# Kernel tuning notes

Hardware: AMD Instinct MI355X
Metric: run time of the kernel (lower is better)

Reference implementation:

```python
import jax, jax.numpy as jnp
import numpy as np


def setup_inputs() -> dict:
    key = jax.random.key(0)
    k1, k2 = jax.random.split(key)
    B, C, H, W = 32, 256, 64, 64
    data = jax.random.normal(k1, (B, C, H, W), dtype=jnp.float32)
    offset = jax.random.normal(k2, (B, 2, H, W), dtype=jnp.float32)
    trans_std = jnp.float32(0.005)  # learned scalar Parameter
    return {"data": data, "offset": offset, "trans_std": trans_std}


def reference(data, offset, trans_std):
    """Offset-driven bilinear interpolation sampling + global average pooling.

    data:   [B, C, H, W]
    offset: [B, 2, H, W]  (dy, dx) displacement field, scaled by trans_std
    Returns pooled features [B, C].
    """
    B, C, H, W = data.shape
    ts = jnp.clip(trans_std, 0.001, 0.01)  # forward clamps trans_std to [0.001, 0.01]

    # sampling coordinates: base grid + scaled offsets (offsets normalized by H/W)
    ii = jnp.arange(H, dtype=data.dtype)[:, None]   # [H,1]
    jj = jnp.arange(W, dtype=data.dtype)[None, :]   # [1,W]
    y = jnp.clip(ii + ts * offset[:, 0] * H, 0.0, H - 1)  # [B,H,W]
    x = jnp.clip(jj + ts * offset[:, 1] * W, 0.0, W - 1)  # [B,H,W]

    y0 = jnp.clip(jnp.floor(y).astype(jnp.int32), 0, H - 2)
    x0 = jnp.clip(jnp.floor(x).astype(jnp.int32), 0, W - 2)
    y1 = y0 + 1
    x1 = x0 + 1
    wy = y - y0.astype(data.dtype)  # [B,H,W] in [0,1]
    wx = x - x0.astype(data.dtype)

    def sample_one(d, yy0, yy1, xx0, xx1):
        # d: [C,H,W]; index maps: [H,W] -> gathered [C,H,W]
        v00 = d[:, yy0, xx0]
        v01 = d[:, yy0, xx1]
        v10 = d[:, yy1, xx0]
        v11 = d[:, yy1, xx1]
        return v00, v01, v10, v11

    v00, v01, v10, v11 = jax.vmap(sample_one)(data, y0, y1, x0, x1)  # each [B,C,H,W]

    wy_ = wy[:, None]  # broadcast over channels -> [B,1,H,W]
    wx_ = wx[:, None]
    sampled = ((1 - wy_) * (1 - wx_) * v00 + (1 - wy_) * wx_ * v01
               + wy_ * (1 - wx_) * v10 + wy_ * wx_ * v11)  # [B,C,H,W]

    # pooling: global average over spatial locations -> [B,C]
    return jnp.mean(sampled, axis=(2, 3))
```

## Files before the change

### kernel.cpp

```cpp
#include <hip/hip_runtime.h>

#define BATCH 32
#define CHAN  256
#define HGT   64
#define WID   64
#define HW    4096

__global__ __launch_bounds__(256) void weight_map_kernel(
        const float* __restrict__ offset,
        const float* __restrict__ ts_ptr,
        float* __restrict__ A)
{
    const int b   = blockIdx.x;
    const int tid = threadIdx.x;

    __shared__ float acc[HW];
    for (int k = tid; k < HW; k += 256) acc[k] = 0.0f;
    __syncthreads();

    float ts = ts_ptr[0];
    ts = fminf(fmaxf(ts, 0.001f), 0.01f);

    const float* off_y = offset + (size_t)b * 2 * HW;
    const float* off_x = off_y + HW;

    for (int p = tid; p < HW; p += 256) {
        const int i = p >> 6;
        const int j = p & 63;
        const float dy = off_y[p];
        const float dx = off_x[p];
        float y = fminf(fmaxf((float)i + ts * dy * 64.0f, 0.0f), 63.0f);
        float x = fminf(fmaxf((float)j + ts * dx * 64.0f, 0.0f), 63.0f);
        int y0 = (int)floorf(y); y0 = min(max(y0, 0), HGT - 2);
        int x0 = (int)floorf(x); x0 = min(max(x0, 0), WID - 2);
        const float wy = y - (float)y0;
        const float wx = x - (float)x0;
        const int base = (y0 << 6) + x0;
        atomicAdd(&acc[base],           (1.0f - wy) * (1.0f - wx));
        atomicAdd(&acc[base + 1],       (1.0f - wy) * wx);
        atomicAdd(&acc[base + WID],     wy * (1.0f - wx));
        atomicAdd(&acc[base + WID + 1], wy * wx);
    }
    __syncthreads();

    float* Ab = A + (size_t)b * HW;
    const float s = 1.0f / (float)HW;
    for (int k = tid; k < HW; k += 256) Ab[k] = acc[k] * s;
}

__global__ __launch_bounds__(256) void dot_kernel(
        const float* __restrict__ data,
        const float* __restrict__ A,
        float* __restrict__ out)
{
    const int blk = blockIdx.x;
    const int b   = blk >> 8;
    const int tid = threadIdx.x;

    const float* plane = data + (size_t)blk * HW;
    const float* Ab    = A    + (size_t)b   * HW;

    float sum = 0.0f;
    #pragma unroll
    for (int it = 0; it < 4; ++it) {
        const int idx = (it * 256 + tid) * 4;
        const float4 dv = *reinterpret_cast<const float4*>(plane + idx);
        const float4 av = *reinterpret_cast<const float4*>(Ab + idx);
        sum = fmaf(av.x, dv.x, sum);
        sum = fmaf(av.y, dv.y, sum);
        sum = fmaf(av.z, dv.z, sum);
        sum = fmaf(av.w, dv.w, sum);
    }

    #pragma unroll
    for (int off = 32; off > 0; off >>= 1)
        sum += __shfl_down(sum, off, 64);

    __shared__ float wsum[4];
    const int lane = tid & 63;
    const int wv   = tid >> 6;
    if (lane == 0) wsum[wv] = sum;
    __syncthreads();
    if (tid == 0) {
        out[blk] = wsum[0] + wsum[1] + wsum[2] + wsum[3];
    }
}

extern "C" void kernel_launch(void* const* d_in, const int* in_sizes, int n_in,
                              void* d_out, int out_size, void* d_ws, size_t ws_size,
                              hipStream_t stream) {
    const float* data   = (const float*)d_in[0];
    const float* offset = (const float*)d_in[1];
    const float* ts     = (const float*)d_in[2];

    float* A   = (float*)d_ws;
    float* out = (float*)d_out;

    weight_map_kernel<<<BATCH, 256, 0, stream>>>(offset, ts, A);
    dot_kernel<<<BATCH * CHAN, 256, 0, stream>>>(data, A, out);
}
```

Measured before the change: 209.8 us.

## Fuse weight-map build and channel dot into one kernel with 8 channels per block

Merges the two kernels into one. Each block rebuilds the per-batch bilinear weight map in shared memory, then dot-products it against 8 channel planes. This removes the second launch, the global round trip of the weight map, and the single-wave serial weight-map kernel that has only 32 blocks. In exchange the weight map, with its shared-memory atomics, is recomputed 32 times per batch, and each block's 16 KB of shared memory may reduce occupancy.

```diff
diff --git a/kernel.cpp b/kernel.cpp
--- a/kernel.cpp
+++ b/kernel.cpp
@@ -5,17 +5,23 @@
 #define HGT   64
 #define WID   64
 #define HW    4096
+#define CPB   8
+#define NBLK  (BATCH * (CHAN / CPB))
 
-__global__ __launch_bounds__(256) void weight_map_kernel(
+__global__ __launch_bounds__(256) void fused_bilinear_pool_kernel(
+        const float* __restrict__ data,
         const float* __restrict__ offset,
         const float* __restrict__ ts_ptr,
-        float* __restrict__ A)
+        float* __restrict__ out)
 {
-    const int b   = blockIdx.x;
     const int tid = threadIdx.x;
+    const int b   = blockIdx.x >> 5;
+    const int g   = blockIdx.x & 31;
 
-    __shared__ float acc[HW];
-    for (int k = tid; k < HW; k += 256) acc[k] = 0.0f;
+    __shared__ float A[HW];
+    __shared__ float red[4 * CPB];
+
+    for (int k = tid; k < HW; k += 256) A[k] = 0.0f;
     __syncthreads();
 
     float ts = ts_ptr[0];
@@ -24,65 +30,72 @@
     const float* off_y = offset + (size_t)b * 2 * HW;
     const float* off_x = off_y + HW;
 
-    for (int p = tid; p < HW; p += 256) {
-        const int i = p >> 6;
-        const int j = p & 63;
-        const float dy = off_y[p];
-        const float dx = off_x[p];
-        float y = fminf(fmaxf((float)i + ts * dy * 64.0f, 0.0f), 63.0f);
-        float x = fminf(fmaxf((float)j + ts * dx * 64.0f, 0.0f), 63.0f);
-        int y0 = (int)floorf(y); y0 = min(max(y0, 0), HGT - 2);
-        int x0 = (int)floorf(x); x0 = min(max(x0, 0), WID - 2);
-        const float wy = y - (float)y0;
-        const float wx = x - (float)x0;
-        const int base = (y0 << 6) + x0;
-        atomicAdd(&acc[base],           (1.0f - wy) * (1.0f - wx));
-        atomicAdd(&acc[base + 1],       (1.0f - wy) * wx);
-        atomicAdd(&acc[base + WID],     wy * (1.0f - wx));
-        atomicAdd(&acc[base + WID + 1], wy * wx);
+    #pragma unroll
+    for (int it = 0; it < 4; ++it) {
+        const int p4 = (it * 256 + tid) * 4;
+        const float4 dy4 = *reinterpret_cast<const float4*>(off_y + p4);
+        const float4 dx4 = *reinterpret_cast<const float4*>(off_x + p4);
+        const float dys[4] = {dy4.x, dy4.y, dy4.z, dy4.w};
+        const float dxs[4] = {dx4.x, dx4.y, dx4.z, dx4.w};
+        #pragma unroll
+        for (int u = 0; u < 4; ++u) {
+            const int p = p4 + u;
+            const int i = p >> 6;
+            const int j = p & 63;
+            float y = fminf(fmaxf((float)i + ts * dys[u] * 64.0f, 0.0f), 63.0f);
+            float x = fminf(fmaxf((float)j + ts * dxs[u] * 64.0f, 0.0f), 63.0f);
+            int y0 = (int)floorf(y); y0 = min(max(y0, 0), HGT - 2);
+            int x0 = (int)floorf(x); x0 = min(max(x0, 0), WID - 2);
+            const float wy = y - (float)y0;
+            const float wx = x - (float)x0;
+            const int base = (y0 << 6) + x0;
+            atomicAdd(&A[base],           (1.0f - wy) * (1.0f - wx));
+            atomicAdd(&A[base + 1],       (1.0f - wy) * wx);
+            atomicAdd(&A[base + WID],     wy * (1.0f - wx));
+            atomicAdd(&A[base + WID + 1], wy * wx);
+        }
     }
     __syncthreads();
 
-    float* Ab = A + (size_t)b * HW;
-    const float s = 1.0f / (float)HW;
-    for (int k = tid; k < HW; k += 256) Ab[k] = acc[k] * s;
-}
+    const float* planes = data + ((size_t)b * CHAN + (size_t)g * CPB) * HW;
 
-__global__ __launch_bounds__(256) void dot_kernel(
-        const float* __restrict__ data,
-        const float* __restrict__ A,
-        float* __restrict__ out)
-{
-    const int blk = blockIdx.x;
-    const int b   = blk >> 8;
-    const int tid = threadIdx.x;
+    float sums[CPB];
+    #pragma unroll
+    for (int c = 0; c < CPB; ++c) sums[c] = 0.0f;
 
-    const float* plane = data + (size_t)blk * HW;
-    const float* Ab    = A    + (size_t)b   * HW;
-
-    float sum = 0.0f;
     #pragma unroll
     for (int it = 0; it < 4; ++it) {
         const int idx = (it * 256 + tid) * 4;
-        const float4 dv = *reinterpret_cast<const float4*>(plane + idx);
-        const float4 av = *reinterpret_cast<const float4*>(Ab + idx);
-        sum = fmaf(av.x, dv.x, sum);
-        sum = fmaf(av.y, dv.y, sum);
-        sum = fmaf(av.z, dv.z, sum);
-        sum = fmaf(av.w, dv.w, sum);
+        const float4 av = *reinterpret_cast<const float4*>(&A[idx]);
+        #pragma unroll
+        for (int c = 0; c < CPB; ++c) {
+            const float4 dv = *reinterpret_cast<const float4*>(planes + (size_t)c * HW + idx);
+            sums[c] = fmaf(av.x, dv.x, sums[c]);
+            sums[c] = fmaf(av.y, dv.y, sums[c]);
+            sums[c] = fmaf(av.z, dv.z, sums[c]);
+            sums[c] = fmaf(av.w, dv.w, sums[c]);
+        }
     }
 
     #pragma unroll
-    for (int off = 32; off > 0; off >>= 1)
-        sum += __shfl_down(sum, off, 64);
-
-    __shared__ float wsum[4];
+    for (int c = 0; c < CPB; ++c) {
+        float s = sums[c];
+        #pragma unroll
+        for (int off = 32; off > 0; off >>= 1)
+            s += __shfl_down(s, off, 64);
+        sums[c] = s;
+    }
     const int lane = tid & 63;
     const int wv   = tid >> 6;
-    if (lane == 0) wsum[wv] = sum;
+    if (lane == 0) {
+        #pragma unroll
+        for (int c = 0; c < CPB; ++c) red[wv * CPB + c] = sums[c];
+    }
     __syncthreads();
-    if (tid == 0) {
-        out[blk] = wsum[0] + wsum[1] + wsum[2] + wsum[3];
+    if (tid < CPB) {
+        const float t = red[0 * CPB + tid] + red[1 * CPB + tid] +
+                        red[2 * CPB + tid] + red[3 * CPB + tid];
+        out[(size_t)b * CHAN + g * CPB + tid] = t * (1.0f / (float)HW);
     }
 }
 
@@ -92,10 +105,7 @@
     const float* data   = (const float*)d_in[0];
     const float* offset = (const float*)d_in[1];
     const float* ts     = (const float*)d_in[2];
-
-    float* A   = (float*)d_ws;
     float* out = (float*)d_out;
 
-    weight_map_kernel<<<BATCH, 256, 0, stream>>>(offset, ts, A);
-    dot_kernel<<<BATCH * CHAN, 256, 0, stream>>>(data, A, out);
+    fused_bilinear_pool_kernel<<<NBLK, 256, 0, stream>>>(data, offset, ts, out);
 }
```

Result: slower. 240.6 us (+14.6%).
